# Optimization experiments

Measured on AMD Instinct MI355X. Metric: run time of the kernel, lower is better.

The kernel has to match this reference:

```python
import jax, jax.numpy as jnp
import numpy as np

N_NODES = 50000
N_EDGES = 640000
D_FEAT = 128
NUM_RELS = 8
EPS = 0.0  # init_eps=0, learn_eps=False -> constant buffer


def setup_inputs() -> dict:
    key = jax.random.key(0)
    k_feat, k_w, k_et, k_src, k_dst = jax.random.split(key, 5)
    feat = jax.random.normal(k_feat, (N_NODES, D_FEAT), dtype=jnp.float32)
    # TypedLinear weight: one [in_feat, out_feat] matrix per relation
    W = jax.random.normal(k_w, (NUM_RELS, D_FEAT, D_FEAT), dtype=jnp.float32) * 0.05
    etypes = jax.random.randint(k_et, (N_EDGES,), 0, NUM_RELS, dtype=jnp.int32)
    src = jax.random.randint(k_src, (N_EDGES,), 0, N_NODES, dtype=jnp.int32)
    dst = jax.random.randint(k_dst, (N_EDGES,), 0, N_NODES, dtype=jnp.int32)
    return {"feat": feat, "W": W, "etypes": etypes, "src": src, "dst": dst}


def reference(feat, W, etypes, src, dst):
    # feat: [N, d]; W: [R, d, d]; etypes/src/dst: [E]
    n_nodes = feat.shape[0]
    num_rels = W.shape[0]
    x = feat[src]  # gather source features, [E, d]
    # TypedLinear: m_e = x_e @ W[etype_e]. Loop over the small fixed relation
    # set (grouped-GEMM form) instead of materializing [E, d, d] weights.
    m = jnp.zeros_like(x)
    for r in range(num_rels):
        mask = (etypes == r)[:, None]
        m = m + jnp.where(mask, x, 0.0) @ W[r]
    # sum aggregation over destination nodes (update_all with fn.sum)
    neigh = jax.ops.segment_sum(m, dst, num_segments=n_nodes)  # [N, d]
    # GIN update: (1 + eps) * h + sum of messages; apply_func/activation are None
    return (1.0 + EPS) * feat + neigh
```

## Files before the change

### kernel.cpp

```cpp
#include <hip/hip_runtime.h>
#include <hip/hip_bf16.h>
#include <stdint.h>

#define D 128

using bf16x8 = __attribute__((ext_vector_type(8))) short;
using f32x4  = __attribute__((ext_vector_type(4))) float;

__device__ __forceinline__ unsigned short f2bf(float f) {
    unsigned u = __float_as_uint(f);
    u = (u + 0x7fffu + ((u >> 16) & 1u)) >> 16;
    return (unsigned short)u;
}
__device__ __forceinline__ float bf2f(unsigned short h) {
    return __uint_as_float(((unsigned)h) << 16);
}

__device__ __forceinline__ bf16x8 cvt8(float4 a, float4 b) {
    union { bf16x8 v; __hip_bfloat162 h[4]; } u;
    u.h[0] = __float22bfloat162_rn(make_float2(a.x, a.y));
    u.h[1] = __float22bfloat162_rn(make_float2(a.z, a.w));
    u.h[2] = __float22bfloat162_rn(make_float2(b.x, b.y));
    u.h[3] = __float22bfloat162_rn(make_float2(b.z, b.w));
    return u.v;
}

__device__ __forceinline__ uint4 pack2(f32x4 x, f32x4 y) {
    union { uint4 u; __hip_bfloat162 h[4]; } o;
    o.h[0] = __float22bfloat162_rn(make_float2(x[0], x[1]));
    o.h[1] = __float22bfloat162_rn(make_float2(x[2], x[3]));
    o.h[2] = __float22bfloat162_rn(make_float2(y[0], y[1]));
    o.h[3] = __float22bfloat162_rn(make_float2(y[2], y[3]));
    return o.u;
}

__global__ __launch_bounds__(256) void prep_kernel(
    const float* __restrict__ feat, unsigned short* __restrict__ featb,
    const float* __restrict__ W, unsigned short* __restrict__ Wt,
    const int* __restrict__ dst, int* __restrict__ deg, int* __restrict__ ord,
    int fcTotal , int wtTotal, int E)
{
    int fcBlocks = (fcTotal + 255) >> 8;
    int wtBlocks = (wtTotal + 255) >> 8;
    int b = blockIdx.x;
    if (b < fcBlocks) {
        int i = b * 256 + threadIdx.x;
        if (i < fcTotal && featb) {
            const float4* p = (const float4*)feat + (size_t)i * 2;
            float4 a = p[0], c = p[1];
            *(bf16x8*)(featb + (size_t)i * 8) = cvt8(a, c);
        }
    } else if (b < fcBlocks + wtBlocks) {
        int idx = (b - fcBlocks) * 256 + threadIdx.x;
        if (idx < wtTotal) {
            int r = idx >> 14;
            int rem = idx & 16383;
            int k = rem >> 7, c = rem & 127;
            Wt[(r << 14) + (c << 7) + k] = f2bf(W[idx]);
        }
    } else {
        int e = (b - fcBlocks - wtBlocks) * 256 + threadIdx.x;
        if (e < E) ord[e] = atomicAdd(&deg[dst[e]], 1);
    }
}

__global__ __launch_bounds__(256) void transform8_kernel(
    const unsigned short* __restrict__ featb, const unsigned short* __restrict__ Wt,
    unsigned short* __restrict__ H, int N)
{
    __shared__ __align__(16) unsigned short sW[128 * 128];
    const int rel  = blockIdx.y;
    const int tid  = threadIdx.x;
    const int wave = tid >> 6, lane = tid & 63;
    const int q    = lane >> 4, mlo = lane & 15;

    {
        const ulonglong2* wsrc = (const ulonglong2*)(Wt + ((size_t)rel << 14));
        #pragma unroll
        for (int i = 0; i < 8; ++i) {
            int idx = tid + 256 * i;
            int row = idx >> 4, ch = idx & 15;
            ulonglong2 v = wsrc[idx];
            *(ulonglong2*)&sW[row * 128 + ((ch ^ (row & 15)) * 8)] = v;
        }
    }

    const int nb = blockIdx.x * 128 + wave * 32;
    bf16x8 bfr[2][4];
    int nodeg[2];
    #pragma unroll
    for (int g = 0; g < 2; ++g) {
        int node = nb + g * 16 + mlo;
        nodeg[g] = node;
        int ld = node < N ? node : N - 1;
        const unsigned short* fp = featb + (size_t)ld * D + q * 8;
        #pragma unroll
        for (int ks = 0; ks < 4; ++ks)
            bfr[g][ks] = *(const bf16x8*)(fp + ks * 32);
    }
    __syncthreads();

    const size_t Hb = (size_t)rel * N * D;
    unsigned short* hp0 = H + Hb + (size_t)nodeg[0] * D + q * 8;
    unsigned short* hp1 = H + Hb + (size_t)nodeg[1] * D + q * 8;

    #pragma unroll
    for (int j = 0; j < 4; ++j) {
        bf16x8 af0[4], af1[4];
        const int row0 = (2 * j) * 16 + mlo, row1 = row0 + 16;
        #pragma unroll
        for (int ks = 0; ks < 4; ++ks) {
            af0[ks] = *(const bf16x8*)&sW[row0 * 128 + (((ks * 4 + q) ^ mlo) * 8)];
            af1[ks] = *(const bf16x8*)&sW[row1 * 128 + (((ks * 4 + q) ^ mlo) * 8)];
        }
        #pragma unroll
        for (int g = 0; g < 2; ++g) {
            f32x4 a = {0.f,0.f,0.f,0.f}, b = {0.f,0.f,0.f,0.f};
            #pragma unroll
            for (int ks = 0; ks < 4; ++ks) {
                a = __builtin_amdgcn_mfma_f32_16x16x32_bf16(af0[ks], bfr[g][ks], a, 0, 0, 0);
                b = __builtin_amdgcn_mfma_f32_16x16x32_bf16(af1[ks], bfr[g][ks], b, 0, 0, 0);
            }
            if (nodeg[g] < N)
                *(uint4*)((g ? hp1 : hp0) + j * 32) = pack2(a, b);
        }
    }
}

__global__ __launch_bounds__(256) void transform8f_kernel(
    const float* __restrict__ feat, const unsigned short* __restrict__ Wt,
    unsigned short* __restrict__ H, int N)
{
    __shared__ __align__(16) unsigned short sW[128 * 128];
    const int rel  = blockIdx.y;
    const int tid  = threadIdx.x;
    const int wave = tid >> 6, lane = tid & 63;
    const int q    = lane >> 4, mlo = lane & 15;

    {
        const ulonglong2* wsrc = (const ulonglong2*)(Wt + ((size_t)rel << 14));
        #pragma unroll
        for (int i = 0; i < 8; ++i) {
            int idx = tid + 256 * i;
            int row = idx >> 4, ch = idx & 15;
            ulonglong2 v = wsrc[idx];
            *(ulonglong2*)&sW[row * 128 + ((ch ^ (row & 15)) * 8)] = v;
        }
    }

    const int nb = blockIdx.x * 128 + wave * 32;
    bf16x8 bfr[2][4];
    int nodeg[2];
    #pragma unroll
    for (int g = 0; g < 2; ++g) {
        int node = nb + g * 16 + mlo;
        nodeg[g] = node;
        int ld = node < N ? node : N - 1;
        const float* fp = feat + (size_t)ld * D + q * 8;
        #pragma unroll
        for (int ks = 0; ks < 4; ++ks)
            bfr[g][ks] = cvt8(*(const float4*)(fp + ks * 32), *(const float4*)(fp + ks * 32 + 4));
    }
    __syncthreads();

    const size_t Hb = (size_t)rel * N * D;
    unsigned short* hp0 = H + Hb + (size_t)nodeg[0] * D + q * 8;
    unsigned short* hp1 = H + Hb + (size_t)nodeg[1] * D + q * 8;

    #pragma unroll
    for (int j = 0; j < 4; ++j) {
        bf16x8 af0[4], af1[4];
        const int row0 = (2 * j) * 16 + mlo, row1 = row0 + 16;
        #pragma unroll
        for (int ks = 0; ks < 4; ++ks) {
            af0[ks] = *(const bf16x8*)&sW[row0 * 128 + (((ks * 4 + q) ^ mlo) * 8)];
            af1[ks] = *(const bf16x8*)&sW[row1 * 128 + (((ks * 4 + q) ^ mlo) * 8)];
        }
        #pragma unroll
        for (int g = 0; g < 2; ++g) {
            f32x4 a = {0.f,0.f,0.f,0.f}, b = {0.f,0.f,0.f,0.f};
            #pragma unroll
            for (int ks = 0; ks < 4; ++ks) {
                a = __builtin_amdgcn_mfma_f32_16x16x32_bf16(af0[ks], bfr[g][ks], a, 0, 0, 0);
                b = __builtin_amdgcn_mfma_f32_16x16x32_bf16(af1[ks], bfr[g][ks], b, 0, 0, 0);
            }
            if (nodeg[g] < N)
                *(uint4*)((g ? hp1 : hp0) + j * 32) = pack2(a, b);
        }
    }
}

__global__ __launch_bounds__(256) void k_blocksum(
    const int* __restrict__ deg, int* __restrict__ part, int N)
{
    int t = threadIdx.x, i = blockIdx.x * 256 + t;
    int v = (i < N) ? deg[i] : 0;
    #pragma unroll
    for (int o = 32; o > 0; o >>= 1) v += __shfl_down(v, o, 64);
    __shared__ int ws_[4];
    if ((t & 63) == 0) ws_[t >> 6] = v;
    __syncthreads();
    if (t == 0) part[blockIdx.x] = ws_[0] + ws_[1] + ws_[2] + ws_[3];
}

__global__ __launch_bounds__(256) void k_scanpart(int* part, int nb)
{
    __shared__ int s[256];
    int t = threadIdx.x;
    int v = (t < nb) ? part[t] : 0;
    s[t] = v;
    #pragma unroll
    for (int o = 1; o < 256; o <<= 1) {
        __syncthreads();
        int x = (t >= o) ? s[t - o] : 0;
        __syncthreads();
        s[t] += x;
    }
    if (t < nb) part[t] = s[t] - v;
}

__global__ __launch_bounds__(256) void k_scanfinal(
    const int* __restrict__ deg, const int* __restrict__ part,
    int* __restrict__ off, int N, int E)
{
    __shared__ int s[256];
    int t = threadIdx.x, i = blockIdx.x * 256 + t;
    int v = (i < N) ? deg[i] : 0;
    s[t] = v;
    #pragma unroll
    for (int o = 1; o < 256; o <<= 1) {
        __syncthreads();
        int x = (t >= o) ? s[t - o] : 0;
        __syncthreads();
        s[t] += x;
    }
    if (i < N) off[i] = part[blockIdx.x] + s[t] - v;
    if (i == 0) off[N] = E;
}

__global__ __launch_bounds__(256) void k_fill(
    const int* __restrict__ dst, const int* __restrict__ et,
    const int* __restrict__ src, const int* __restrict__ off,
    const int* __restrict__ ord, unsigned int* __restrict__ sorted, int E, int N)
{
    int e = blockIdx.x * 256 + threadIdx.x;
    if (e >= E) return;
    unsigned key = ((unsigned)et[e] * (unsigned)N + (unsigned)src[e]) << 8;
    sorted[off[dst[e]] + ord[e]] = key;
}

__global__ __launch_bounds__(256) void k_gather4(
    const char* __restrict__ Hc, const unsigned int* __restrict__ sorted,
    const int* __restrict__ off, const float* __restrict__ feat,
    float* __restrict__ out, int N)
{
    int n = blockIdx.x * 4 + (threadIdx.x >> 6);
    if (n >= N) return;
    int lane = threadIdx.x & 63;

    const int jj = lane >> 4, qq = (lane >> 2) & 3, pp = lane & 3;
    const int f = 16 * jj + 8 * (pp >> 1) + 2 * qq + (pp & 1);

    float2 acc = ((const float2*)feat)[(size_t)n * 64 + f];

    int j0 = __builtin_amdgcn_readfirstlane(off[n]);
    int j1 = __builtin_amdgcn_readfirstlane(off[n + 1]);
    int deg = j1 - j0;
    if (deg > 0) {
        unsigned ep = sorted[j0 + (lane < deg ? lane : deg - 1)];
        int capped = deg < 64 ? deg : 64;
        for (int done = 0; done < capped; done += 16) {
            unsigned a[16];
            #pragma unroll
            for (int u = 0; u < 16; ++u) {
                int idx = done + u; idx = idx < capped ? idx : capped - 1;
                unsigned p = __shfl(ep, idx);
                a[u] = *(const unsigned*)(Hc + p + lane * 4);
            }
            #pragma unroll
            for (int u = 0; u < 16; ++u) {
                bool v = (done + u) < capped;
                acc.x += v ? bf2f((unsigned short)(a[u] & 0xffffu)) : 0.f;
                acc.y += v ? bf2f((unsigned short)(a[u] >> 16)) : 0.f;
            }
        }
        for (int j = j0 + 64; j < j1; ++j) {
            unsigned p = sorted[j];
            unsigned a0 = *(const unsigned*)(Hc + p + lane * 4);
            acc.x += bf2f((unsigned short)(a0 & 0xffffu));
            acc.y += bf2f((unsigned short)(a0 >> 16));
        }
    }
    ((float2*)out)[(size_t)n * 64 + f] = acc;
}

__global__ __launch_bounds__(256) void init_kernel(
    const float* __restrict__ feat, float* __restrict__ out, int n4)
{
    int i = blockIdx.x * 256 + threadIdx.x;
    if (i < n4) ((float4*)out)[i] = ((const float4*)feat)[i];
}

__global__ __launch_bounds__(128) void edge_matvec_kernel(
    const float* __restrict__ feat, const float* __restrict__ W,
    const int* __restrict__ et, const int* __restrict__ src,
    const int* __restrict__ dst, float* __restrict__ out, int E)
{
    __shared__ float xs[D];
    int e = blockIdx.x;
    int c = threadIdx.x;
    int s = src[e], r = et[e], d = dst[e];
    xs[c] = feat[(size_t)s * D + c];
    __syncthreads();
    const float* Wr = W + (size_t)r * D * D;
    float acc = 0.f;
    #pragma unroll 8
    for (int k = 0; k < D; ++k) acc += xs[k] * Wr[(size_t)k * D + c];
    atomicAdd(out + (size_t)d * D + c, acc);
}

static inline size_t al256(size_t x) { return (x + 255) & ~(size_t)255; }

extern "C" void kernel_launch(void* const* d_in, const int* in_sizes, int n_in,
                              void* d_out, int out_size, void* d_ws, size_t ws_size,
                              hipStream_t stream) {
    const float* feat = (const float*)d_in[0];
    const float* W    = (const float*)d_in[1];
    const int*   et   = (const int*)d_in[2];
    const int*   src  = (const int*)d_in[3];
    const int*   dst  = (const int*)d_in[4];
    float* out = (float*)d_out;

    const int N = in_sizes[0] / D;
    const int R = in_sizes[1] / (D * D);
    const int E = in_sizes[2];

    size_t hB   = al256((size_t)R * N * D * sizeof(unsigned short));
    size_t wtB  = al256((size_t)R * D * D * sizeof(unsigned short));
    size_t offB = al256((size_t)(N + 1) * sizeof(int));
    size_t degB = al256((size_t)N * sizeof(int));
    size_t ordB = al256((size_t)E * sizeof(int));
    size_t parB = al256(1024 * sizeof(int));
    size_t srtB = al256((size_t)E * sizeof(unsigned int));
    size_t fbB  = al256((size_t)N * D * sizeof(unsigned short));
    size_t need_base = hB + wtB + offB + degB + ordB + parB + srtB;
    size_t need_full = need_base + fbB;

    const int nbScan = (N + 255) / 256;
    const bool packable = (nbScan <= 256) &&
                          ((size_t)R * (size_t)N * 256ull <= 0xFFFFFFFFull);

    if (ws_size >= need_base && packable) {
        char* p = (char*)d_ws;
        unsigned short* H      = (unsigned short*)p;           p += hB;
        unsigned short* Wt     = (unsigned short*)p;           p += wtB;
        int*            off    = (int*)p;                      p += offB;
        int*            deg    = (int*)p;                      p += degB;
        int*            ord    = (int*)p;                      p += ordB;
        int*            part   = (int*)p;                      p += parB;
        unsigned int*   sorted = (unsigned int*)p;             p += srtB;
        unsigned short* featb  = (ws_size >= need_full) ? (unsigned short*)p : nullptr;

        int wtTotal = R * D * D;
        int fcTotal = featb ? (N * D) / 8 : 0;
        int fcBlocks = (fcTotal + 255) / 256;
        int wtBlocks = (wtTotal + 255) / 256;
        int cntBlocks = (E + 255) / 256;

        hipMemsetAsync(deg, 0, (size_t)N * sizeof(int), stream);
        prep_kernel<<<fcBlocks + wtBlocks + cntBlocks, 256, 0, stream>>>(
            feat, featb, W, Wt, dst, deg, ord, fcTotal, wtTotal, E);

        dim3 tg((N + 127) / 128, R);
        if (featb)
            transform8_kernel<<<tg, 256, 0, stream>>>(featb, Wt, H, N);
        else
            transform8f_kernel<<<tg, 256, 0, stream>>>(feat, Wt, H, N);

        k_blocksum<<<nbScan, 256, 0, stream>>>(deg, part, N);
        k_scanpart<<<1, 256, 0, stream>>>(part, nbScan);
        k_scanfinal<<<nbScan, 256, 0, stream>>>(deg, part, off, N, E);
        k_fill<<<cntBlocks, 256, 0, stream>>>(dst, et, src, off, ord, sorted, E, N);

        k_gather4<<<(N + 3) / 4, 256, 0, stream>>>((const char*)H, sorted, off, feat, out, N);
    } else {
        int n4 = (N * D) / 4;
        init_kernel<<<(n4 + 255) / 256, 256, 0, stream>>>(feat, out, n4);
        edge_matvec_kernel<<<E, 128, 0, stream>>>(feat, W, et, src, dst, out, E);
    }
}
```

Measured before the change: 196.9 us.

## Fuse degree counting into transform kernel and drop bf16 feature copy

```diff
diff --git a/kernel.cpp b/kernel.cpp
--- a/kernel.cpp
+++ b/kernel.cpp
@@ -34,42 +34,34 @@
     return o.u;
 }
 
-__global__ __launch_bounds__(256) void prep_kernel(
-    const float* __restrict__ feat, unsigned short* __restrict__ featb,
-    const float* __restrict__ W, unsigned short* __restrict__ Wt,
+__global__ __launch_bounds__(256) void prep_wt_kernel(
+    const float* __restrict__ W, unsigned short* __restrict__ Wt, int total)
+{
+    int idx = blockIdx.x * 256 + threadIdx.x;
+    if (idx >= total) return;
+    int r = idx >> 14;
+    int rem = idx & 16383;
+    int k = rem >> 7, c = rem & 127;
+    Wt[(r << 14) + (c << 7) + k] = f2bf(W[idx]);
+}
+
+__global__ __launch_bounds__(256) void fused_transform_count_kernel(
+    const float* __restrict__ feat, const unsigned short* __restrict__ Wt,
+    unsigned short* __restrict__ H,
     const int* __restrict__ dst, int* __restrict__ deg, int* __restrict__ ord,
-    int fcTotal , int wtTotal, int E)
-{
-    int fcBlocks = (fcTotal + 255) >> 8;
-    int wtBlocks = (wtTotal + 255) >> 8;
-    int b = blockIdx.x;
-    if (b < fcBlocks) {
-        int i = b * 256 + threadIdx.x;
-        if (i < fcTotal && featb) {
-            const float4* p = (const float4*)feat + (size_t)i * 2;
-            float4 a = p[0], c = p[1];
-            *(bf16x8*)(featb + (size_t)i * 8) = cvt8(a, c);
-        }
-    } else if (b < fcBlocks + wtBlocks) {
-        int idx = (b - fcBlocks) * 256 + threadIdx.x;
-        if (idx < wtTotal) {
-            int r = idx >> 14;
-            int rem = idx & 16383;
-            int k = rem >> 7, c = rem & 127;
-            Wt[(r << 14) + (c << 7) + k] = f2bf(W[idx]);
-        }
-    } else {
-        int e = (b - fcBlocks - wtBlocks) * 256 + threadIdx.x;
+    int N, int NBX, int tBlocks, int E)
+{
+    __shared__ __align__(16) unsigned short sW[128 * 128];
+    const int b = blockIdx.x;
+
+    if (b >= tBlocks) {
+        int e = (b - tBlocks) * 256 + threadIdx.x;
         if (e < E) ord[e] = atomicAdd(&deg[dst[e]], 1);
-    }
-}
-
-__global__ __launch_bounds__(256) void transform8_kernel(
-    const unsigned short* __restrict__ featb, const unsigned short* __restrict__ Wt,
-    unsigned short* __restrict__ H, int N)
-{
-    __shared__ __align__(16) unsigned short sW[128 * 128];
-    const int rel  = blockIdx.y;
+        return;
+    }
+
+    const int rel = b / NBX;
+    const int bx  = b - rel * NBX;
     const int tid  = threadIdx.x;
     const int wave = tid >> 6, lane = tid & 63;
     const int q    = lane >> 4, mlo = lane & 15;
@@ -85,70 +77,7 @@
         }
     }
 
-    const int nb = blockIdx.x * 128 + wave * 32;
-    bf16x8 bfr[2][4];
-    int nodeg[2];
-    #pragma unroll
-    for (int g = 0; g < 2; ++g) {
-        int node = nb + g * 16 + mlo;
-        nodeg[g] = node;
-        int ld = node < N ? node : N - 1;
-        const unsigned short* fp = featb + (size_t)ld * D + q * 8;
-        #pragma unroll
-        for (int ks = 0; ks < 4; ++ks)
-            bfr[g][ks] = *(const bf16x8*)(fp + ks * 32);
-    }
-    __syncthreads();
-
-    const size_t Hb = (size_t)rel * N * D;
-    unsigned short* hp0 = H + Hb + (size_t)nodeg[0] * D + q * 8;
-    unsigned short* hp1 = H + Hb + (size_t)nodeg[1] * D + q * 8;
-
-    #pragma unroll
-    for (int j = 0; j < 4; ++j) {
-        bf16x8 af0[4], af1[4];
-        const int row0 = (2 * j) * 16 + mlo, row1 = row0 + 16;
-        #pragma unroll
-        for (int ks = 0; ks < 4; ++ks) {
-            af0[ks] = *(const bf16x8*)&sW[row0 * 128 + (((ks * 4 + q) ^ mlo) * 8)];
-            af1[ks] = *(const bf16x8*)&sW[row1 * 128 + (((ks * 4 + q) ^ mlo) * 8)];
-        }
-        #pragma unroll
-        for (int g = 0; g < 2; ++g) {
-            f32x4 a = {0.f,0.f,0.f,0.f}, b = {0.f,0.f,0.f,0.f};
-            #pragma unroll
-            for (int ks = 0; ks < 4; ++ks) {
-                a = __builtin_amdgcn_mfma_f32_16x16x32_bf16(af0[ks], bfr[g][ks], a, 0, 0, 0);
-                b = __builtin_amdgcn_mfma_f32_16x16x32_bf16(af1[ks], bfr[g][ks], b, 0, 0, 0);
-            }
-            if (nodeg[g] < N)
-                *(uint4*)((g ? hp1 : hp0) + j * 32) = pack2(a, b);
-        }
-    }
-}
-
-__global__ __launch_bounds__(256) void transform8f_kernel(
-    const float* __restrict__ feat, const unsigned short* __restrict__ Wt,
-    unsigned short* __restrict__ H, int N)
-{
-    __shared__ __align__(16) unsigned short sW[128 * 128];
-    const int rel  = blockIdx.y;
-    const int tid  = threadIdx.x;
-    const int wave = tid >> 6, lane = tid & 63;
-    const int q    = lane >> 4, mlo = lane & 15;
-
-    {
-        const ulonglong2* wsrc = (const ulonglong2*)(Wt + ((size_t)rel << 14));
-        #pragma unroll
-        for (int i = 0; i < 8; ++i) {
-            int idx = tid + 256 * i;
-            int row = idx >> 4, ch = idx & 15;
-            ulonglong2 v = wsrc[idx];
-            *(ulonglong2*)&sW[row * 128 + ((ch ^ (row & 15)) * 8)] = v;
-        }
-    }
-
-    const int nb = blockIdx.x * 128 + wave * 32;
+    const int nb = bx * 128 + wave * 32;
     bf16x8 bfr[2][4];
     int nodeg[2];
     #pragma unroll
@@ -178,14 +107,14 @@
         }
         #pragma unroll
         for (int g = 0; g < 2; ++g) {
-            f32x4 a = {0.f,0.f,0.f,0.f}, b = {0.f,0.f,0.f,0.f};
+            f32x4 a = {0.f,0.f,0.f,0.f}, c = {0.f,0.f,0.f,0.f};
             #pragma unroll
             for (int ks = 0; ks < 4; ++ks) {
                 a = __builtin_amdgcn_mfma_f32_16x16x32_bf16(af0[ks], bfr[g][ks], a, 0, 0, 0);
-                b = __builtin_amdgcn_mfma_f32_16x16x32_bf16(af1[ks], bfr[g][ks], b, 0, 0, 0);
+                c = __builtin_amdgcn_mfma_f32_16x16x32_bf16(af1[ks], bfr[g][ks], c, 0, 0, 0);
             }
             if (nodeg[g] < N)
-                *(uint4*)((g ? hp1 : hp0) + j * 32) = pack2(a, b);
+                *(uint4*)((g ? hp1 : hp0) + j * 32) = pack2(a, c);
         }
     }
 }
@@ -342,15 +271,13 @@
     size_t ordB = al256((size_t)E * sizeof(int));
     size_t parB = al256(1024 * sizeof(int));
     size_t srtB = al256((size_t)E * sizeof(unsigned int));
-    size_t fbB  = al256((size_t)N * D * sizeof(unsigned short));
-    size_t need_base = hB + wtB + offB + degB + ordB + parB + srtB;
-    size_t need_full = need_base + fbB;
+    size_t need = hB + wtB + offB + degB + ordB + parB + srtB;
 
     const int nbScan = (N + 255) / 256;
     const bool packable = (nbScan <= 256) &&
                           ((size_t)R * (size_t)N * 256ull <= 0xFFFFFFFFull);
 
-    if (ws_size >= need_base && packable) {
+    if (ws_size >= need && packable) {
         char* p = (char*)d_ws;
         unsigned short* H      = (unsigned short*)p;           p += hB;
         unsigned short* Wt     = (unsigned short*)p;           p += wtB;
@@ -358,24 +285,18 @@
         int*            deg    = (int*)p;                      p += degB;
         int*            ord    = (int*)p;                      p += ordB;
         int*            part   = (int*)p;                      p += parB;
-        unsigned int*   sorted = (unsigned int*)p;             p += srtB;
-        unsigned short* featb  = (ws_size >= need_full) ? (unsigned short*)p : nullptr;
+        unsigned int*   sorted = (unsigned int*)p;
 
         int wtTotal = R * D * D;
-        int fcTotal = featb ? (N * D) / 8 : 0;
-        int fcBlocks = (fcTotal + 255) / 256;
-        int wtBlocks = (wtTotal + 255) / 256;
         int cntBlocks = (E + 255) / 256;
 
         hipMemsetAsync(deg, 0, (size_t)N * sizeof(int), stream);
-        prep_kernel<<<fcBlocks + wtBlocks + cntBlocks, 256, 0, stream>>>(
-            feat, featb, W, Wt, dst, deg, ord, fcTotal, wtTotal, E);
-
-        dim3 tg((N + 127) / 128, R);
-        if (featb)
-            transform8_kernel<<<tg, 256, 0, stream>>>(featb, Wt, H, N);
-        else
-            transform8f_kernel<<<tg, 256, 0, stream>>>(feat, Wt, H, N);
+        prep_wt_kernel<<<(wtTotal + 255) / 256, 256, 0, stream>>>(W, Wt, wtTotal);
+
+        int NBX = (N + 127) / 128;
+        int tBlocks = NBX * R;
+        fused_transform_count_kernel<<<tBlocks + cntBlocks, 256, 0, stream>>>(
+            feat, Wt, H, dst, deg, ord, N, NBX, tBlocks, E);
 
         k_blocksum<<<nbScan, 256, 0, stream>>>(deg, part, N);
         k_scanpart<<<1, 256, 0, stream>>>(part, nbScan);
```

Result: slower. 201.8 us (+2.5%).
